# Kernel optimization log

Hardware: AMD Instinct MI355X
Metric: run time of the kernel (lower is better)

Reference implementation:

```python
import jax, jax.numpy as jnp
import numpy as np

Q_DIM, KV_DIM, H = 64, 64, 4


def setup_inputs() -> dict:
    key = jax.random.key(0)
    ks = jax.random.split(key, 8)
    b, t = 8, 128
    q_x = jax.random.normal(ks[0], (b, t, Q_DIM), dtype=jnp.float32)
    kv_x = jax.random.normal(ks[1], (b, t, t - 1, KV_DIM), dtype=jnp.float32)
    # nn.Linear weights: (out_features, in_features), applied as x @ W.T
    Wk = jax.random.normal(ks[2], (KV_DIM * H, KV_DIM), dtype=jnp.float32) * 0.05
    Wq = jax.random.normal(ks[3], (KV_DIM * H, Q_DIM), dtype=jnp.float32) * 0.05
    Wv = jax.random.normal(ks[4], (KV_DIM * H, KV_DIM), dtype=jnp.float32) * 0.05
    bias = jax.random.uniform(ks[5], (KV_DIM,), minval=-0.1, maxval=0.1, dtype=jnp.float32)
    Ws = jax.random.normal(ks[6], (1, KV_DIM), dtype=jnp.float32) * 0.05
    bs = jax.random.normal(ks[7], (1,), dtype=jnp.float32) * 0.05
    return {"q_x": q_x, "kv_x": kv_x, "Wk": Wk, "Wq": Wq, "Wv": Wv,
            "bias": bias, "Ws": Ws, "bs": bs}


def reference(q_x, kv_x, Wk, Wq, Wv, bias, Ws, bs):
    b, t, tm1, k = kv_x.shape  # tm1 == t-1
    h = H
    # keys: (b, t, t-1, h, k)
    keys = (kv_x @ Wk.T).reshape(b, t, tm1, h, k)
    # queries: (b, t, 1, h, k)
    queries = (q_x @ Wq.T).reshape(b, t, 1, h, k)
    # additive tanh score projected to scalar per (b,t,n,h)
    act = jnp.tanh(keys + queries + bias)
    score = jnp.einsum('btnhk,k->btnh', act, Ws[0]) + bs[0]
    # softmax over the t-1 key axis (dim=2)
    w = jax.nn.softmax(score, axis=2)  # (b, t, t-1, h)
    values = (kv_x @ Wv.T).reshape(b, t, tm1, h, k)
    # weighted sum over t-1
    x = jnp.einsum('btnh,btnhk->bthk', w, values)
    return x.reshape(b, t, h * k)
```

## Files before the change

### kernel.cpp

```cpp
#include <hip/hip_runtime.h>
#include <math.h>

#define B 8
#define T 128
#define NKEY 127
#define NPAD 128
#define KDIM 64
#define NH 4
#define CH 256

typedef short short8 __attribute__((ext_vector_type(8)));
typedef float floatx4 __attribute__((ext_vector_type(4)));

__device__ __forceinline__ float fast_tanh(float x) {
    float e = __expf(2.f * x);
    float r = __builtin_amdgcn_rcpf(e + 1.f);
    return fmaf(-2.f, r, 1.f);
}

__device__ __forceinline__ void rne8(const float4& a, const float4& b, short8& hi) {
    float x[8] = {a.x, a.y, a.z, a.w, b.x, b.y, b.z, b.w};
    #pragma unroll
    for (int i = 0; i < 8; ++i) {
        unsigned u = __float_as_uint(x[i]);
        u += 0x7FFFu + ((u >> 16) & 1u);
        hi[i] = (short)(u >> 16);
    }
}

__global__ __launch_bounds__(256, 2)
void attn_kernel(const float* __restrict__ q_x,
                 const float* __restrict__ kv_x,
                 const float* __restrict__ Wk,
                 const float* __restrict__ Wq,
                 const float* __restrict__ Wv,
                 const float* __restrict__ bias,
                 const float* __restrict__ Ws,
                 const float* __restrict__ bs,
                 float* __restrict__ out)
{
    __shared__ __align__(16) short bh_lds[16][64][8];
    __shared__ float qb_lds[CH];
    __shared__ float p_lds[NH][NPAD];
    __shared__ __align__(16) float wkv_lds[NH][KDIM];

    const int bt   = blockIdx.x;
    const int tid  = threadIdx.x;
    const int h    = tid >> 6;
    const int lane = tid & 63;
    const int col  = lane & 15;
    const int quad = lane >> 4;

    const float* __restrict__ kvg = kv_x + (size_t)bt * NKEY * KDIM;

    #pragma unroll
    for (int w = 0; w < 4; ++w) {
        const int chunk = w * 4 + h;
        const int nt = chunk >> 1, ks = chunk & 1;
        const int n  = nt * 16 + (lane & 15);
        const int k0 = ks * 32 + (lane >> 4) * 8;
        float4 a = make_float4(0.f, 0.f, 0.f, 0.f);
        float4 b = make_float4(0.f, 0.f, 0.f, 0.f);
        if (n < NKEY) {
            const float* p = kvg + (size_t)n * KDIM + k0;
            a = *(const float4*)p;
            b = *(const float4*)(p + 4);
        }
        short8 hi;
        rne8(a, b, hi);
        *(short8*)&bh_lds[chunk][lane][0] = hi;
    }

    {
        const float4* Wq4 = (const float4*)(Wq + (size_t)tid * KDIM);
        const float4* q4g = (const float4*)(q_x + (size_t)bt * KDIM);
        float4 qa = {0.f, 0.f, 0.f, 0.f};
        #pragma unroll
        for (int i = 0; i < 16; ++i) {
            float4 w = Wq4[i];
            float4 q4 = q4g[i];
            qa.x = fmaf(q4.x, w.x, qa.x);
            qa.y = fmaf(q4.y, w.y, qa.y);
            qa.z = fmaf(q4.z, w.z, qa.z);
            qa.w = fmaf(q4.w, w.w, qa.w);
        }
        qb_lds[tid] = (qa.x + qa.y) + (qa.z + qa.w) + bias[tid & 63];
    }

    short8 ahi[4][2];
    #pragma unroll
    for (int jt = 0; jt < 4; ++jt)
        #pragma unroll
        for (int ks = 0; ks < 2; ++ks) {
            const float* wrow = Wk + (size_t)(h * 64 + jt * 16 + col) * KDIM
                                   + ks * 32 + quad * 8;
            float4 a = *(const float4*)wrow;
            float4 b = *(const float4*)(wrow + 4);
            rne8(a, b, ahi[jt][ks]);
        }

    __syncthreads();

    float qbv[4][4], wsv[4][4];
    #pragma unroll
    for (int jt = 0; jt < 4; ++jt)
        #pragma unroll
        for (int r = 0; r < 4; ++r) {
            int j = jt * 16 + quad * 4 + r;
            qbv[jt][r] = qb_lds[h * 64 + j];
            wsv[jt][r] = Ws[j];
        }

    #pragma unroll
    for (int nt = 0; nt < 8; ++nt) {
        short8 bhi0 = *(const short8*)&bh_lds[nt * 2 + 0][lane][0];
        short8 bhi1 = *(const short8*)&bh_lds[nt * 2 + 1][lane][0];

        floatx4 acc[4];
        #pragma unroll
        for (int jt = 0; jt < 4; ++jt) {
            floatx4 c = {0.f, 0.f, 0.f, 0.f};
            c = __builtin_amdgcn_mfma_f32_16x16x32_bf16(ahi[jt][0], bhi0, c, 0, 0, 0);
            c = __builtin_amdgcn_mfma_f32_16x16x32_bf16(ahi[jt][1], bhi1, c, 0, 0, 0);
            acc[jt] = c;
        }

        float partial = 0.f;
        #pragma unroll
        for (int jt = 0; jt < 4; ++jt)
            #pragma unroll
            for (int r = 0; r < 4; ++r)
                partial = fmaf(fast_tanh(acc[jt][r] + qbv[jt][r]), wsv[jt][r], partial);
        partial += __shfl_xor(partial, 16, 64);
        partial += __shfl_xor(partial, 32, 64);
        if (lane < 16) p_lds[h][nt * 16 + lane] = partial;
    }

    float invl;
    {
        float s_a = p_lds[h][lane];
        float s_b = p_lds[h][64 + lane];
        if (lane == 63) s_b = -1e30f;
        float mx = fmaxf(s_a, s_b);
        #pragma unroll
        for (int off = 32; off > 0; off >>= 1)
            mx = fmaxf(mx, __shfl_xor(mx, off, 64));
        float pa = __expf(s_a - mx);
        float pb = __expf(s_b - mx);
        float ls = pa + pb;
        #pragma unroll
        for (int off = 32; off > 0; off >>= 1)
            ls += __shfl_xor(ls, off, 64);
        invl = 1.f / ls;
        p_lds[h][lane]      = pa;
        p_lds[h][64 + lane] = pb;
    }

    {
        float4 a4 = make_float4(0.f, 0.f, 0.f, 0.f);
        #pragma unroll
        for (int i = 0; i < 31; ++i) {
            const int n = 4 * i + quad;
            float4 v = *(const float4*)&kvg[(size_t)n * KDIM + 4 * col];
            const float pn = p_lds[h][n];
            a4.x = fmaf(pn, v.x, a4.x);
            a4.y = fmaf(pn, v.y, a4.y);
            a4.z = fmaf(pn, v.z, a4.z);
            a4.w = fmaf(pn, v.w, a4.w);
        }
        {
            const int n = 124 + quad;
            const int n_eff = (n < NKEY) ? n : 0;
            float4 v = *(const float4*)&kvg[(size_t)n_eff * KDIM + 4 * col];
            const float pn = p_lds[h][n];
            a4.x = fmaf(pn, v.x, a4.x);
            a4.y = fmaf(pn, v.y, a4.y);
            a4.z = fmaf(pn, v.z, a4.z);
            a4.w = fmaf(pn, v.w, a4.w);
        }
        a4.x += __shfl_xor(a4.x, 16, 64);  a4.y += __shfl_xor(a4.y, 16, 64);
        a4.z += __shfl_xor(a4.z, 16, 64);  a4.w += __shfl_xor(a4.w, 16, 64);
        a4.x += __shfl_xor(a4.x, 32, 64);  a4.y += __shfl_xor(a4.y, 32, 64);
        a4.z += __shfl_xor(a4.z, 32, 64);  a4.w += __shfl_xor(a4.w, 32, 64);
        if (lane < 16) {
            float4 r = make_float4(a4.x * invl, a4.y * invl, a4.z * invl, a4.w * invl);
            *(float4*)&wkv_lds[h][4 * col] = r;
        }
    }

    {
        const float4* Wv4 = (const float4*)(Wv + (size_t)tid * KDIM);
        const float4* wv_row = (const float4*)wkv_lds[h];
        float4 oa = {0.f, 0.f, 0.f, 0.f};
        #pragma unroll
        for (int i = 0; i < 16; ++i) {
            float4 w = Wv4[i];
            float4 c = wv_row[i];
            oa.x = fmaf(c.x, w.x, oa.x);
            oa.y = fmaf(c.y, w.y, oa.y);
            oa.z = fmaf(c.z, w.z, oa.z);
            oa.w = fmaf(c.w, w.w, oa.w);
        }
        out[(size_t)bt * CH + tid] = (oa.x + oa.y) + (oa.z + oa.w);
    }
}

extern "C" void kernel_launch(void* const* d_in, const int* in_sizes, int n_in,
                              void* d_out, int out_size, void* d_ws, size_t ws_size,
                              hipStream_t stream) {
    const float* q_x  = (const float*)d_in[0];
    const float* kv_x = (const float*)d_in[1];
    const float* Wk   = (const float*)d_in[2];
    const float* Wq   = (const float*)d_in[3];
    const float* Wv   = (const float*)d_in[4];
    const float* bias = (const float*)d_in[5];
    const float* Ws   = (const float*)d_in[6];
    const float* bs   = (const float*)d_in[7];
    float* out = (float*)d_out;

    attn_kernel<<<dim3(B * T), dim3(256), 0, stream>>>(
        q_x, kv_x, Wk, Wq, Wv, bias, Ws, bs, out);
}
```

Baseline: 117.7 us.

## Split each head across two waves with 512-thread blocks

Doubles the block to 8 waves so each head is handled by two waves, each covering half of the key tiles for scores and half of the keys for the weighted value sum. Partial value sums are combined in LDS before the Wv projection, and the softmax normalisation moves to the final output scale. Wk fragments are loaded in two passes to cut register pressure, and launch bounds ask for higher occupancy. In exchange it adds extra block-wide barriers and leaves half the threads idle during the Wq and Wv projections.

```diff
diff --git a/kernel.cpp b/kernel.cpp
--- a/kernel.cpp
+++ b/kernel.cpp
@@ -28,7 +28,7 @@
     }
 }
 
-__global__ __launch_bounds__(256, 2)
+__global__ __launch_bounds__(512, 8)
 void attn_kernel(const float* __restrict__ q_x,
                  const float* __restrict__ kv_x,
                  const float* __restrict__ Wk,
@@ -42,23 +42,26 @@
     __shared__ __align__(16) short bh_lds[16][64][8];
     __shared__ float qb_lds[CH];
     __shared__ float p_lds[NH][NPAD];
-    __shared__ __align__(16) float wkv_lds[NH][KDIM];
+    __shared__ __align__(16) float part_lds[NH][2][KDIM];
+    __shared__ float invl_lds[NH];
 
     const int bt   = blockIdx.x;
     const int tid  = threadIdx.x;
-    const int h    = tid >> 6;
+    const int w    = tid >> 6;
     const int lane = tid & 63;
+    const int h    = w >> 1;
+    const int half = w & 1;
     const int col  = lane & 15;
     const int quad = lane >> 4;
 
     const float* __restrict__ kvg = kv_x + (size_t)bt * NKEY * KDIM;
 
     #pragma unroll
-    for (int w = 0; w < 4; ++w) {
-        const int chunk = w * 4 + h;
+    for (int c = 0; c < 2; ++c) {
+        const int chunk = c * 8 + w;
         const int nt = chunk >> 1, ks = chunk & 1;
-        const int n  = nt * 16 + (lane & 15);
-        const int k0 = ks * 32 + (lane >> 4) * 8;
+        const int n  = nt * 16 + col;
+        const int k0 = ks * 32 + quad * 8;
         float4 a = make_float4(0.f, 0.f, 0.f, 0.f);
         float4 b = make_float4(0.f, 0.f, 0.f, 0.f);
         if (n < NKEY) {
@@ -71,73 +74,74 @@
         *(short8*)&bh_lds[chunk][lane][0] = hi;
     }
 
-    {
+    if (tid < CH) {
         const float4* Wq4 = (const float4*)(Wq + (size_t)tid * KDIM);
         const float4* q4g = (const float4*)(q_x + (size_t)bt * KDIM);
         float4 qa = {0.f, 0.f, 0.f, 0.f};
         #pragma unroll
         for (int i = 0; i < 16; ++i) {
-            float4 w = Wq4[i];
+            float4 ww = Wq4[i];
             float4 q4 = q4g[i];
-            qa.x = fmaf(q4.x, w.x, qa.x);
-            qa.y = fmaf(q4.y, w.y, qa.y);
-            qa.z = fmaf(q4.z, w.z, qa.z);
-            qa.w = fmaf(q4.w, w.w, qa.w);
+            qa.x = fmaf(q4.x, ww.x, qa.x);
+            qa.y = fmaf(q4.y, ww.y, qa.y);
+            qa.z = fmaf(q4.z, ww.z, qa.z);
+            qa.w = fmaf(q4.w, ww.w, qa.w);
         }
         qb_lds[tid] = (qa.x + qa.y) + (qa.z + qa.w) + bias[tid & 63];
     }
 
-    short8 ahi[4][2];
-    #pragma unroll
-    for (int jt = 0; jt < 4; ++jt)
-        #pragma unroll
-        for (int ks = 0; ks < 2; ++ks) {
-            const float* wrow = Wk + (size_t)(h * 64 + jt * 16 + col) * KDIM
-                                   + ks * 32 + quad * 8;
-            float4 a = *(const float4*)wrow;
-            float4 b = *(const float4*)(wrow + 4);
-            rne8(a, b, ahi[jt][ks]);
-        }
-
-    __syncthreads();
-
-    float qbv[4][4], wsv[4][4];
-    #pragma unroll
-    for (int jt = 0; jt < 4; ++jt)
-        #pragma unroll
-        for (int r = 0; r < 4; ++r) {
-            int j = jt * 16 + quad * 4 + r;
-            qbv[jt][r] = qb_lds[h * 64 + j];
-            wsv[jt][r] = Ws[j];
-        }
-
-    #pragma unroll
-    for (int nt = 0; nt < 8; ++nt) {
-        short8 bhi0 = *(const short8*)&bh_lds[nt * 2 + 0][lane][0];
-        short8 bhi1 = *(const short8*)&bh_lds[nt * 2 + 1][lane][0];
-
-        floatx4 acc[4];
-        #pragma unroll
-        for (int jt = 0; jt < 4; ++jt) {
-            floatx4 c = {0.f, 0.f, 0.f, 0.f};
-            c = __builtin_amdgcn_mfma_f32_16x16x32_bf16(ahi[jt][0], bhi0, c, 0, 0, 0);
-            c = __builtin_amdgcn_mfma_f32_16x16x32_bf16(ahi[jt][1], bhi1, c, 0, 0, 0);
-            acc[jt] = c;
-        }
-
-        float partial = 0.f;
-        #pragma unroll
-        for (int jt = 0; jt < 4; ++jt)
+    __syncthreads();
+
+    float sp[4] = {0.f, 0.f, 0.f, 0.f};
+    #pragma unroll
+    for (int pass = 0; pass < 2; ++pass) {
+        short8 ahi[2][2];
+        float qbp[2][4], wsp[2][4];
+        #pragma unroll
+        for (int jj = 0; jj < 2; ++jj) {
+            const int jt = pass * 2 + jj;
             #pragma unroll
-            for (int r = 0; r < 4; ++r)
-                partial = fmaf(fast_tanh(acc[jt][r] + qbv[jt][r]), wsv[jt][r], partial);
-        partial += __shfl_xor(partial, 16, 64);
-        partial += __shfl_xor(partial, 32, 64);
-        if (lane < 16) p_lds[h][nt * 16 + lane] = partial;
-    }
-
-    float invl;
-    {
+            for (int ks = 0; ks < 2; ++ks) {
+                const float* wrow = Wk + (size_t)(h * 64 + jt * 16 + col) * KDIM
+                                       + ks * 32 + quad * 8;
+                float4 a = *(const float4*)wrow;
+                float4 b = *(const float4*)(wrow + 4);
+                rne8(a, b, ahi[jj][ks]);
+            }
+            #pragma unroll
+            for (int r = 0; r < 4; ++r) {
+                const int j = jt * 16 + quad * 4 + r;
+                qbp[jj][r] = qb_lds[h * 64 + j];
+                wsp[jj][r] = Ws[j];
+            }
+        }
+        #pragma unroll
+        for (int ntl = 0; ntl < 4; ++ntl) {
+            const int nt = half * 4 + ntl;
+            short8 b0 = *(const short8*)&bh_lds[nt * 2 + 0][lane][0];
+            short8 b1 = *(const short8*)&bh_lds[nt * 2 + 1][lane][0];
+            #pragma unroll
+            for (int jj = 0; jj < 2; ++jj) {
+                floatx4 c = {0.f, 0.f, 0.f, 0.f};
+                c = __builtin_amdgcn_mfma_f32_16x16x32_bf16(ahi[jj][0], b0, c, 0, 0, 0);
+                c = __builtin_amdgcn_mfma_f32_16x16x32_bf16(ahi[jj][1], b1, c, 0, 0, 0);
+                #pragma unroll
+                for (int r = 0; r < 4; ++r)
+                    sp[ntl] = fmaf(fast_tanh(c[r] + qbp[jj][r]), wsp[jj][r], sp[ntl]);
+            }
+        }
+    }
+    #pragma unroll
+    for (int ntl = 0; ntl < 4; ++ntl) {
+        float s = sp[ntl];
+        s += __shfl_xor(s, 16, 64);
+        s += __shfl_xor(s, 32, 64);
+        if (lane < 16) p_lds[h][(half * 4 + ntl) * 16 + lane] = s;
+    }
+
+    __syncthreads();
+
+    if (half == 0) {
         float s_a = p_lds[h][lane];
         float s_b = p_lds[h][64 + lane];
         if (lane == 63) s_b = -1e30f;
@@ -151,25 +155,18 @@
         #pragma unroll
         for (int off = 32; off > 0; off >>= 1)
             ls += __shfl_xor(ls, off, 64);
-        invl = 1.f / ls;
         p_lds[h][lane]      = pa;
         p_lds[h][64 + lane] = pb;
-    }
+        if (lane == 0) invl_lds[h] = 1.f / ls;
+    }
+
+    __syncthreads();
 
     {
         float4 a4 = make_float4(0.f, 0.f, 0.f, 0.f);
         #pragma unroll
-        for (int i = 0; i < 31; ++i) {
-            const int n = 4 * i + quad;
-            float4 v = *(const float4*)&kvg[(size_t)n * KDIM + 4 * col];
-            const float pn = p_lds[h][n];
-            a4.x = fmaf(pn, v.x, a4.x);
-            a4.y = fmaf(pn, v.y, a4.y);
-            a4.z = fmaf(pn, v.z, a4.z);
-            a4.w = fmaf(pn, v.w, a4.w);
-        }
-        {
-            const int n = 124 + quad;
+        for (int i = 0; i < 16; ++i) {
+            const int n = half * 64 + 4 * i + quad;
             const int n_eff = (n < NKEY) ? n : 0;
             float4 v = *(const float4*)&kvg[(size_t)n_eff * KDIM + 4 * col];
             const float pn = p_lds[h][n];
@@ -182,26 +179,33 @@
         a4.z += __shfl_xor(a4.z, 16, 64);  a4.w += __shfl_xor(a4.w, 16, 64);
         a4.x += __shfl_xor(a4.x, 32, 64);  a4.y += __shfl_xor(a4.y, 32, 64);
         a4.z += __shfl_xor(a4.z, 32, 64);  a4.w += __shfl_xor(a4.w, 32, 64);
-        if (lane < 16) {
-            float4 r = make_float4(a4.x * invl, a4.y * invl, a4.z * invl, a4.w * invl);
-            *(float4*)&wkv_lds[h][4 * col] = r;
-        }
-    }
-
-    {
-        const float4* Wv4 = (const float4*)(Wv + (size_t)tid * KDIM);
-        const float4* wv_row = (const float4*)wkv_lds[h];
+        if (lane < 16)
+            *(float4*)&part_lds[h][half][4 * col] = a4;
+    }
+
+    __syncthreads();
+
+    if (tid < CH) {
+        const int j  = tid;
+        const int hh = j >> 6;
+        const float inv = invl_lds[hh];
+        const float4* Wv4 = (const float4*)(Wv + (size_t)j * KDIM);
+        const float4* p0  = (const float4*)part_lds[hh][0];
+        const float4* p1  = (const float4*)part_lds[hh][1];
         float4 oa = {0.f, 0.f, 0.f, 0.f};
         #pragma unroll
         for (int i = 0; i < 16; ++i) {
-            float4 w = Wv4[i];
-            float4 c = wv_row[i];
-            oa.x = fmaf(c.x, w.x, oa.x);
-            oa.y = fmaf(c.y, w.y, oa.y);
-            oa.z = fmaf(c.z, w.z, oa.z);
-            oa.w = fmaf(c.w, w.w, oa.w);
-        }
-        out[(size_t)bt * CH + tid] = (oa.x + oa.y) + (oa.z + oa.w);
+            float4 ww = Wv4[i];
+            float4 c0 = p0[i];
+            float4 c1 = p1[i];
+            float cx = c0.x + c1.x, cy = c0.y + c1.y;
+            float cz = c0.z + c1.z, cw = c0.w + c1.w;
+            oa.x = fmaf(cx, ww.x, oa.x);
+            oa.y = fmaf(cy, ww.y, oa.y);
+            oa.z = fmaf(cz, ww.z, oa.z);
+            oa.w = fmaf(cw, ww.w, oa.w);
+        }
+        out[(size_t)bt * CH + j] = ((oa.x + oa.y) + (oa.z + oa.w)) * inv;
     }
 }
 
@@ -218,6 +222,6 @@
     const float* bs   = (const float*)d_in[7];
     float* out = (float*)d_out;
 
-    attn_kernel<<<dim3(B * T), dim3(256), 0, stream>>>(
+    attn_kernel<<<dim3(B * T), dim3(512), 0, stream>>>(
         q_x, kv_x, Wk, Wq, Wv, bias, Ws, bs, out);
 }
```

Result: slower. 176.5 us (+49.9%).
